# Optimization experiments

Hardware: AMD Instinct MI355X
Metric: run time of the kernel (lower is better)

The kernel has to match this reference:

```python
import jax, jax.numpy as jnp
import numpy as np
from jax import lax

T, B, INPUT_DIM, RNN_DIM = 512, 64, 512, 512
STDV = 1.0 / np.sqrt(float(RNN_DIM))


def setup_inputs() -> dict:
    key = jax.random.key(0)
    k0, k1, k2, k3 = jax.random.split(key, 4)
    input_vectors = jax.random.normal(k0, (T, B, INPUT_DIM), dtype=jnp.float32)
    # params mimic reset_parameters: uniform(-stdv, stdv), stdv = 1/sqrt(rnn_dim)
    weight = jax.random.uniform(k1, (INPUT_DIM + RNN_DIM, RNN_DIM), dtype=jnp.float32, minval=-STDV, maxval=STDV)
    bias = jax.random.uniform(k2, (1, RNN_DIM), dtype=jnp.float32, minval=-STDV, maxval=STDV)
    init_hidden = jax.random.uniform(k3, (1, RNN_DIM), dtype=jnp.float32, minval=-STDV, maxval=STDV)
    return {"input_vectors": input_vectors, "weight": weight, "bias": bias, "init_hidden": init_hidden}


def reference(input_vectors, weight, bias, init_hidden):
    # direction='l'. Output at step i is the hidden state BEFORE the i-th update
    # (the torch code appends prev_hidden before computing new_hidden).
    batch = input_vectors.shape[1]
    rnn_dim = init_hidden.shape[1]
    h0 = jnp.broadcast_to(init_hidden, (batch, rnn_dim))

    def step(h, x):  # h: [B, R], x: [B, D]
        new_h = jnp.tanh(jnp.concatenate([x, h], axis=1) @ weight + bias)
        return new_h, h  # emit pre-update hidden, carry post-update

    _, seq_hidden = lax.scan(step, h0, input_vectors)  # [T, B, R]
    return seq_hidden
```

## Files before the change

### kernel.cpp

```cpp
#include <hip/hip_runtime.h>
#include <hip/hip_bf16.h>
#include <hip/hip_fp16.h>

#define T_STEPS 512
#define BATCH   64
#define DIM     512
#define ROWS    16

typedef _Float16 half2_t __attribute__((ext_vector_type(2)));
typedef _Float16 half8_t __attribute__((ext_vector_type(8)));
typedef short    bf16x8 __attribute__((ext_vector_type(8)));
typedef float    f32x4  __attribute__((ext_vector_type(4)));

static __device__ __forceinline__ unsigned short f2bf(float f) {
    union { float f; unsigned u; } v; v.f = f;
    unsigned r = v.u + 0x7fffu + ((v.u >> 16) & 1u);
    return (unsigned short)(r >> 16);
}

static __device__ __forceinline__ float fast_tanh(float x) {
    float e = __expf(2.0f * x);
    return 1.0f - 2.0f * __builtin_amdgcn_rcpf(e + 1.0f);
}

__global__ __launch_bounds__(256) void tr_cvt_kernel(const float* __restrict__ src,
                                                     unsigned short* __restrict__ dst) {
    __shared__ float tile[32][33];
    const int bx = blockIdx.x * 32;
    const int by = blockIdx.y * 32;
    const int tx = threadIdx.x;
    const int ty = threadIdx.y;
    #pragma unroll
    for (int i = ty; i < 32; i += 8)
        tile[i][tx] = src[(size_t)(by + i) * DIM + (bx + tx)];
    __syncthreads();
    #pragma unroll
    for (int i = ty; i < 32; i += 8)
        dst[(size_t)(bx + i) * DIM + (by + tx)] = f2bf(tile[tx][i]);
}

__global__ __launch_bounds__(256) void tr_cvt_f16_kernel(const float* __restrict__ src,
                                                         _Float16* __restrict__ dst) {
    __shared__ float tile[32][33];
    const int bx = blockIdx.x * 32;
    const int by = blockIdx.y * 32;
    const int tx = threadIdx.x;
    const int ty = threadIdx.y;
    #pragma unroll
    for (int i = ty; i < 32; i += 8)
        tile[i][tx] = src[(size_t)(by + i) * DIM + (bx + tx)];
    __syncthreads();
    #pragma unroll
    for (int i = ty; i < 32; i += 8)
        dst[(size_t)(bx + i) * DIM + (by + tx)] = (_Float16)tile[tx][i];
}

__global__ __launch_bounds__(256) void gemm_z_kernel(const float* __restrict__ X,
                                                     const unsigned short* __restrict__ WxT,
                                                     const float* __restrict__ bias,
                                                     _Float16* __restrict__ Zo) {
    const int bm   = blockIdx.y;
    const int bn   = blockIdx.x;
    const int wave = threadIdx.x >> 6;
    const int lane = threadIdx.x & 63;
    const int mBase = bm * 128 + (wave >> 1) * 64;
    const int nBase = bn * 128 + (wave & 1) * 64;
    const int l15 = lane & 15;
    const int q   = lane >> 4;
    f32x4 acc[4][4] = {};
    for (int kt = 0; kt < 512; kt += 32) {
        const int kk = kt + q * 8;
        bf16x8 a[4], b[4];
        #pragma unroll
        for (int i = 0; i < 4; ++i) {
            const float* ap = X + (size_t)(mBase + i * 16 + l15) * DIM + kk;
            float4 f0 = *(const float4*)(ap);
            float4 f1 = *(const float4*)(ap + 4);
            bf16x8 av;
            av[0] = (short)f2bf(f0.x); av[1] = (short)f2bf(f0.y);
            av[2] = (short)f2bf(f0.z); av[3] = (short)f2bf(f0.w);
            av[4] = (short)f2bf(f1.x); av[5] = (short)f2bf(f1.y);
            av[6] = (short)f2bf(f1.z); av[7] = (short)f2bf(f1.w);
            a[i] = av;
        }
        #pragma unroll
        for (int i = 0; i < 4; ++i)
            b[i] = *(const bf16x8*)(WxT + (size_t)(nBase + i * 16 + l15) * DIM + kk);
        #pragma unroll
        for (int mi = 0; mi < 4; ++mi)
            #pragma unroll
            for (int ni = 0; ni < 4; ++ni)
                acc[mi][ni] = __builtin_amdgcn_mfma_f32_16x16x32_bf16(a[mi], b[ni], acc[mi][ni], 0, 0, 0);
    }
    #pragma unroll
    for (int ni = 0; ni < 4; ++ni) {
        const int col = nBase + ni * 16 + l15;
        const float bv = bias[col];
        const int w_ = col >> 6, ct_ = (col >> 4) & 3, l15_ = col & 15;
        #pragma unroll
        for (int mi = 0; mi < 4; ++mi) {
            #pragma unroll
            for (int rg = 0; rg < 4; ++rg) {
                const int row = mBase + mi * 16 + q * 4 + rg;
                const int t_ = row >> 6, brow = row & 63;
                const int b_ = brow >> 4, r4 = brow & 15;
                const int l_ = (r4 >> 2) * 16 + l15_;
                const int i_ = ct_ * 4 + (r4 & 3);
                Zo[(size_t)t_ * 32768 + (size_t)((b_ * 8 + w_) * 64 + l_) * 16 + i_] =
                    (_Float16)(acc[mi][ni][rg] + bv);
            }
        }
    }
}

__global__ __launch_bounds__(512, 2) void rnn_mfma_kernel(const _Float16* __restrict__ Zw,
                                                          const _Float16* __restrict__ WhT,
                                                          const float* __restrict__ h0,
                                                          float* __restrict__ out) {
    __shared__ _Float16 WlA[65536];
    __shared__ _Float16 Ah[8192];
    const int tid = threadIdx.x;
    const int w = tid >> 6, l = tid & 63;
    const int l15 = l & 15, q = l >> 4;
    const int b = blockIdx.x;
    const int wbase = w * 64;

    half8_t bw[12][4];
    #pragma unroll
    for (int kt = 0; kt < 12; ++kt)
        #pragma unroll
        for (int ct = 0; ct < 4; ++ct)
            bw[kt][ct] = *(const half8_t*)(WhT + (size_t)(wbase + ct * 16 + l15) * DIM + kt * 32 + q * 8);
    #pragma unroll
    for (int kt = 0; kt < 12; ++kt)
        #pragma unroll
        for (int ct = 0; ct < 4; ++ct)
            asm volatile("" : "+v"(bw[kt][ct]));
    #pragma unroll
    for (int ktl = 0; ktl < 4; ++ktl)
        #pragma unroll
        for (int ct = 0; ct < 4; ++ct) {
            half8_t v = *(const half8_t*)(WhT + (size_t)(wbase + ct * 16 + l15) * DIM + (12 + ktl) * 32 + q * 8);
            *(half8_t*)(WlA + (size_t)((w * 16 + ct * 4 + ktl) * 512 + l * 8)) = v;
        }

    const int hi = l15 >> 3, l7 = l15 & 7;
    const int abase = w * 1024 + hi * 32 + q * 8 + l7;
    float* p0 = out + (size_t)(b * 16 + q * 4) * DIM + wbase + l15;
    float h0c[4];
    #pragma unroll
    for (int ct = 0; ct < 4; ++ct) h0c[ct] = h0[wbase + ct * 16 + l15];
    #pragma unroll
    for (int ct = 0; ct < 4; ++ct)
        #pragma unroll
        for (int rg = 0; rg < 4; ++rg) {
            p0[rg * DIM + ct * 16] = h0c[ct];
            Ah[abase + (ct >> 1) * 512 + (ct & 1) * 64 + rg * 128] = (_Float16)h0c[ct];
        }
    __syncthreads();

    const int aslot = (l & 3) * 128 + (l >> 2) * 8;
    const _Float16* pz = Zw + ((size_t)(b * 8 + w) * 64 + l) * 16;
    half8_t z0 = *(const half8_t*)(pz);
    half8_t z1 = *(const half8_t*)(pz + 8);
    float* pout = out + (size_t)(BATCH + b * 16 + q * 4) * DIM + wbase + l15;

    for (int t = 0; t < T_STEPS - 1; ++t) {
        f32x4 acc[4];
        #pragma unroll
        for (int ct = 0; ct < 4; ++ct)
            #pragma unroll
            for (int rg = 0; rg < 4; ++rg) {
                const int i = ct * 4 + rg;
                acc[ct][rg] = (float)(i < 8 ? z0[i] : z1[i - 8]);
            }
        half8_t zn0 = *(const half8_t*)(pz + (size_t)(t + 1) * 32768);
        half8_t zn1 = *(const half8_t*)(pz + (size_t)(t + 1) * 32768 + 8);

        #pragma unroll
        for (int kt = 0; kt < 12; ++kt) {
            half8_t af = *(const half8_t*)(Ah + kt * 512 + aslot);
            #pragma unroll
            for (int ct = 0; ct < 4; ++ct)
                acc[ct] = __builtin_amdgcn_mfma_f32_16x16x32_f16(af, bw[kt][ct], acc[ct], 0, 0, 0);
        }
        #pragma unroll
        for (int ktl = 0; ktl < 4; ++ktl) {
            half8_t af = *(const half8_t*)(Ah + (12 + ktl) * 512 + aslot);
            #pragma unroll
            for (int ct = 0; ct < 4; ++ct) {
                half8_t wf = *(const half8_t*)(WlA + (size_t)((w * 16 + ct * 4 + ktl) * 512 + l * 8));
                acc[ct] = __builtin_amdgcn_mfma_f32_16x16x32_f16(af, wf, acc[ct], 0, 0, 0);
            }
        }
        asm volatile("s_waitcnt lgkmcnt(0)\n\ts_barrier" ::: "memory");
        #pragma unroll
        for (int ct = 0; ct < 4; ++ct)
            #pragma unroll
            for (int rg = 0; rg < 4; ++rg) {
                const float hv = fast_tanh(acc[ct][rg]);
                pout[rg * DIM + ct * 16] = hv;
                Ah[abase + (ct >> 1) * 512 + (ct & 1) * 64 + rg * 128] = (_Float16)hv;
            }
        asm volatile("s_waitcnt lgkmcnt(0)\n\ts_barrier" ::: "memory");
        pout += BATCH * DIM;
        z0 = zn0; z1 = zn1;
    }
}

extern "C" void kernel_launch(void* const* d_in, const int* in_sizes, int n_in,
                              void* d_out, int out_size, void* d_ws, size_t ws_size,
                              hipStream_t stream) {
    const float* X    = (const float*)d_in[0];
    const float* W    = (const float*)d_in[1];
    const float* bias = (const float*)d_in[2];
    const float* h0   = (const float*)d_in[3];
    float* out = (float*)d_out;

    char* ws = (char*)d_ws;
    unsigned short* WxT = (unsigned short*)(ws);
    _Float16*       WhT = (_Float16*)(ws + 524288);
    _Float16*       Zws = (_Float16*)(ws + 1048576);

    dim3 tb(32, 8);
    tr_cvt_kernel<<<dim3(16, 16), tb, 0, stream>>>(W, WxT);
    tr_cvt_f16_kernel<<<dim3(16, 16), tb, 0, stream>>>(W + 512 * 512, WhT);
    gemm_z_kernel<<<dim3(4, 256), 256, 0, stream>>>(X, WxT, bias, Zws);
    rnn_mfma_kernel<<<4, 512, 0, stream>>>(Zws, WhT, h0, out);
}
```

Measured before the change: 1.197 ms.

## Double-buffer hidden state in LDS with XOR swizzle and single barrier per step

The hidden-state LDS buffer is now double-buffered: each step reads from one buffer and writes the new tanh outputs to the other. This removes one of the two workgroup barriers per timestep on the serial recurrence. The A-fragment layout is also changed to an XOR-swizzled slot pattern to reduce LDS bank conflicts, and s_setprio raises wave priority around the MFMA section. In exchange the kernel uses twice the LDS for the hidden state and has more complex address arithmetic.

```diff
diff --git a/kernel.cpp b/kernel.cpp
--- a/kernel.cpp
+++ b/kernel.cpp
@@ -5,7 +5,6 @@
 #define T_STEPS 512
 #define BATCH   64
 #define DIM     512
-#define ROWS    16
 
 typedef _Float16 half2_t __attribute__((ext_vector_type(2)));
 typedef _Float16 half8_t __attribute__((ext_vector_type(8)));
@@ -118,10 +117,11 @@
                                                           const float* __restrict__ h0,
                                                           float* __restrict__ out) {
     __shared__ _Float16 WlA[65536];
-    __shared__ _Float16 Ah[8192];
+    __shared__ _Float16 Ah2[2][8192];
     const int tid = threadIdx.x;
     const int w = tid >> 6, l = tid & 63;
     const int l15 = l & 15, q = l >> 4;
+    const int hi = l15 >> 3, l7 = l15 & 7;
     const int b = blockIdx.x;
     const int wbase = w * 64;
 
@@ -144,28 +144,31 @@
             *(half8_t*)(WlA + (size_t)((w * 16 + ct * 4 + ktl) * 512 + l * 8)) = v;
         }
 
-    const int hi = l15 >> 3, l7 = l15 & 7;
-    const int abase = w * 1024 + hi * 32 + q * 8 + l7;
     float* p0 = out + (size_t)(b * 16 + q * 4) * DIM + wbase + l15;
-    float h0c[4];
-    #pragma unroll
-    for (int ct = 0; ct < 4; ++ct) h0c[ct] = h0[wbase + ct * 16 + l15];
-    #pragma unroll
-    for (int ct = 0; ct < 4; ++ct)
+    #pragma unroll
+    for (int ct = 0; ct < 4; ++ct) {
+        const float hv = h0[wbase + ct * 16 + l15];
+        const int ktc = w * 2 + (ct >> 1);
+        const int Lb  = ((ct & 1) * 2 + hi) * 16 + q * 4;
         #pragma unroll
         for (int rg = 0; rg < 4; ++rg) {
-            p0[rg * DIM + ct * 16] = h0c[ct];
-            Ah[abase + (ct >> 1) * 512 + (ct & 1) * 64 + rg * 128] = (_Float16)h0c[ct];
-        }
+            p0[rg * DIM + ct * 16] = hv;
+            const int L = Lb + rg;
+            const int ps = L ^ (L >> 2);
+            Ah2[0][ktc * 512 + ps * 8 + l7] = (_Float16)hv;
+        }
+    }
     __syncthreads();
 
-    const int aslot = (l & 3) * 128 + (l >> 2) * 8;
+    const int psl = (l ^ (l >> 2)) * 8;
     const _Float16* pz = Zw + ((size_t)(b * 8 + w) * 64 + l) * 16;
     half8_t z0 = *(const half8_t*)(pz);
     half8_t z1 = *(const half8_t*)(pz + 8);
     float* pout = out + (size_t)(BATCH + b * 16 + q * 4) * DIM + wbase + l15;
 
     for (int t = 0; t < T_STEPS - 1; ++t) {
+        const _Float16* Ahr = Ah2[t & 1];
+        _Float16*       Ahw = Ah2[(t + 1) & 1];
         f32x4 acc[4];
         #pragma unroll
         for (int ct = 0; ct < 4; ++ct)
@@ -177,34 +180,51 @@
         half8_t zn0 = *(const half8_t*)(pz + (size_t)(t + 1) * 32768);
         half8_t zn1 = *(const half8_t*)(pz + (size_t)(t + 1) * 32768 + 8);
 
+        __builtin_amdgcn_s_setprio(1);
         #pragma unroll
         for (int kt = 0; kt < 12; ++kt) {
-            half8_t af = *(const half8_t*)(Ah + kt * 512 + aslot);
+            half8_t af = *(const half8_t*)(Ahr + kt * 512 + psl);
             #pragma unroll
             for (int ct = 0; ct < 4; ++ct)
                 acc[ct] = __builtin_amdgcn_mfma_f32_16x16x32_f16(af, bw[kt][ct], acc[ct], 0, 0, 0);
         }
         #pragma unroll
         for (int ktl = 0; ktl < 4; ++ktl) {
-            half8_t af = *(const half8_t*)(Ah + (12 + ktl) * 512 + aslot);
+            half8_t af = *(const half8_t*)(Ahr + (12 + ktl) * 512 + psl);
             #pragma unroll
             for (int ct = 0; ct < 4; ++ct) {
                 half8_t wf = *(const half8_t*)(WlA + (size_t)((w * 16 + ct * 4 + ktl) * 512 + l * 8));
                 acc[ct] = __builtin_amdgcn_mfma_f32_16x16x32_f16(af, wf, acc[ct], 0, 0, 0);
             }
         }
+        __builtin_amdgcn_s_setprio(0);
+
+        float hv[4][4];
+        #pragma unroll
+        for (int ct = 0; ct < 4; ++ct)
+            #pragma unroll
+            for (int rg = 0; rg < 4; ++rg)
+                hv[ct][rg] = fast_tanh(acc[ct][rg]);
+        #pragma unroll
+        for (int ct = 0; ct < 4; ++ct) {
+            const int ktc = w * 2 + (ct >> 1);
+            const int Lb  = ((ct & 1) * 2 + hi) * 16 + q * 4;
+            #pragma unroll
+            for (int rg = 0; rg < 4; ++rg) {
+                const int L = Lb + rg;
+                const int ps = L ^ (L >> 2);
+                Ahw[ktc * 512 + ps * 8 + l7] = (_Float16)hv[ct][rg];
+            }
+        }
+        #pragma unroll
+        for (int ct = 0; ct < 4; ++ct)
+            #pragma unroll
+            for (int rg = 0; rg < 4; ++rg)
+                pout[rg * DIM + ct * 16] = hv[ct][rg];
+
+        z0 = zn0; z1 = zn1;
+        pout += BATCH * DIM;
         asm volatile("s_waitcnt lgkmcnt(0)\n\ts_barrier" ::: "memory");
-        #pragma unroll
-        for (int ct = 0; ct < 4; ++ct)
-            #pragma unroll
-            for (int rg = 0; rg < 4; ++rg) {
-                const float hv = fast_tanh(acc[ct][rg]);
-                pout[rg * DIM + ct * 16] = hv;
-                Ah[abase + (ct >> 1) * 512 + (ct & 1) * 64 + rg * 128] = (_Float16)hv;
-            }
-        asm volatile("s_waitcnt lgkmcnt(0)\n\ts_barrier" ::: "memory");
-        pout += BATCH * DIM;
-        z0 = zn0; z1 = zn1;
     }
 }
 
```

After: 1.306 ms. 1.09x slower.

## Double-buffer hidden state, swap MFMA operands, stream weight tail from global

Applied to the files above, without the earlier changes.

Double-buffers the fp16 hidden-state LDS tile so each step needs one barrier instead of two. It also swaps the MFMA operand order so each lane holds four consecutive output columns, which allows vectorized float4 output stores and half4 LDS writes with an XOR-swizzled layout. The last four K tiles of the recurrent weight are now re-read from global/L2 every step instead of from a large LDS copy, and a dummy LDS pad limits occupancy. It also raises wave priority around the MFMA chain, adding per-step global weight traffic in exchange for less LDS use and fewer syncs.

```diff
diff --git a/kernel.cpp b/kernel.cpp
--- a/kernel.cpp
+++ b/kernel.cpp
@@ -5,9 +5,11 @@
 #define T_STEPS 512
 #define BATCH   64
 #define DIM     512
-#define ROWS    16
+#define REG_KT  12
+#define STR_KT  4
 
 typedef _Float16 half2_t __attribute__((ext_vector_type(2)));
+typedef _Float16 half4_t __attribute__((ext_vector_type(4)));
 typedef _Float16 half8_t __attribute__((ext_vector_type(8)));
 typedef short    bf16x8 __attribute__((ext_vector_type(8)));
 typedef float    f32x4  __attribute__((ext_vector_type(4)));
@@ -96,17 +98,19 @@
     for (int ni = 0; ni < 4; ++ni) {
         const int col = nBase + ni * 16 + l15;
         const float bv = bias[col];
-        const int w_ = col >> 6, ct_ = (col >> 4) & 3, l15_ = col & 15;
+        const int w_  = col >> 6;
+        const int c64 = col & 63;
+        const int ct_ = c64 >> 4;
+        const int q_  = (c64 & 15) >> 2;
+        const int rg_ = c64 & 3;
         #pragma unroll
         for (int mi = 0; mi < 4; ++mi) {
             #pragma unroll
             for (int rg = 0; rg < 4; ++rg) {
                 const int row = mBase + mi * 16 + q * 4 + rg;
-                const int t_ = row >> 6, brow = row & 63;
-                const int b_ = brow >> 4, r4 = brow & 15;
-                const int l_ = (r4 >> 2) * 16 + l15_;
-                const int i_ = ct_ * 4 + (r4 & 3);
-                Zo[(size_t)t_ * 32768 + (size_t)((b_ * 8 + w_) * 64 + l_) * 16 + i_] =
+                const int t_ = row >> 6, batch = row & 63;
+                const int b_ = batch >> 4, l15k = batch & 15;
+                Zo[(size_t)t_ * 32768 + (size_t)((b_ * 8 + w_) * 64 + (q_ * 16 + l15k)) * 16 + ct_ * 4 + rg_] =
                     (_Float16)(acc[mi][ni][rg] + bv);
             }
         }
@@ -117,55 +121,63 @@
                                                           const _Float16* __restrict__ WhT,
                                                           const float* __restrict__ h0,
                                                           float* __restrict__ out) {
-    __shared__ _Float16 WlA[65536];
-    __shared__ _Float16 Ah[8192];
+    __shared__ _Float16 Ah2[2][8192];
+    __shared__ half8_t  lds_pad[3600];
     const int tid = threadIdx.x;
     const int w = tid >> 6, l = tid & 63;
     const int l15 = l & 15, q = l >> 4;
     const int b = blockIdx.x;
     const int wbase = w * 64;
 
-    half8_t bw[12][4];
-    #pragma unroll
-    for (int kt = 0; kt < 12; ++kt)
+    ((volatile _Float16*)lds_pad)[tid] = (_Float16)0.f;
+
+    half8_t bw[REG_KT][4];
+    #pragma unroll
+    for (int kt = 0; kt < REG_KT; ++kt)
         #pragma unroll
         for (int ct = 0; ct < 4; ++ct)
             bw[kt][ct] = *(const half8_t*)(WhT + (size_t)(wbase + ct * 16 + l15) * DIM + kt * 32 + q * 8);
     #pragma unroll
-    for (int kt = 0; kt < 12; ++kt)
+    for (int kt = 0; kt < REG_KT; ++kt)
         #pragma unroll
         for (int ct = 0; ct < 4; ++ct)
             asm volatile("" : "+v"(bw[kt][ct]));
-    #pragma unroll
-    for (int ktl = 0; ktl < 4; ++ktl)
-        #pragma unroll
-        for (int ct = 0; ct < 4; ++ct) {
-            half8_t v = *(const half8_t*)(WhT + (size_t)(wbase + ct * 16 + l15) * DIM + (12 + ktl) * 32 + q * 8);
-            *(half8_t*)(WlA + (size_t)((w * 16 + ct * 4 + ktl) * 512 + l * 8)) = v;
-        }
-
-    const int hi = l15 >> 3, l7 = l15 & 7;
-    const int abase = w * 1024 + hi * 32 + q * 8 + l7;
-    float* p0 = out + (size_t)(b * 16 + q * 4) * DIM + wbase + l15;
-    float h0c[4];
-    #pragma unroll
-    for (int ct = 0; ct < 4; ++ct) h0c[ct] = h0[wbase + ct * 16 + l15];
+
+    const _Float16* pw[4];
     #pragma unroll
     for (int ct = 0; ct < 4; ++ct)
-        #pragma unroll
-        for (int rg = 0; rg < 4; ++rg) {
-            p0[rg * DIM + ct * 16] = h0c[ct];
-            Ah[abase + (ct >> 1) * 512 + (ct & 1) * 64 + rg * 128] = (_Float16)h0c[ct];
-        }
+        pw[ct] = WhT + (size_t)(wbase + ct * 16 + l15) * DIM + REG_KT * 32 + q * 8;
+
+    int aw_off[4];
+    #pragma unroll
+    for (int ct = 0; ct < 4; ++ct) {
+        const int kt = w * 2 + (ct >> 1);
+        const int Lt = ((ct & 1) * 2 + (q >> 1)) * 16 + l15;
+        const int ps = Lt ^ (Lt >> 2);
+        aw_off[ct] = kt * 512 + ps * 8 + (q & 1) * 4;
+    }
+
+    float* p0 = out + (size_t)(b * 16 + l15) * DIM + wbase + q * 4;
+    #pragma unroll
+    for (int ct = 0; ct < 4; ++ct) {
+        const float4 hv = *(const float4*)(h0 + wbase + ct * 16 + q * 4);
+        *(float4*)(p0 + ct * 16) = hv;
+        half4_t hh;
+        hh[0] = (_Float16)hv.x; hh[1] = (_Float16)hv.y;
+        hh[2] = (_Float16)hv.z; hh[3] = (_Float16)hv.w;
+        *(half4_t*)(&Ah2[0][0] + aw_off[ct]) = hh;
+    }
     __syncthreads();
 
-    const int aslot = (l & 3) * 128 + (l >> 2) * 8;
+    const int psl = (l ^ (l >> 2)) * 8;
     const _Float16* pz = Zw + ((size_t)(b * 8 + w) * 64 + l) * 16;
     half8_t z0 = *(const half8_t*)(pz);
     half8_t z1 = *(const half8_t*)(pz + 8);
-    float* pout = out + (size_t)(BATCH + b * 16 + q * 4) * DIM + wbase + l15;
+    float* pout = out + (size_t)(BATCH + b * 16 + l15) * DIM + wbase + q * 4;
 
     for (int t = 0; t < T_STEPS - 1; ++t) {
+        const _Float16* Ahr = Ah2[t & 1];
+        _Float16*       Ahw = Ah2[(t + 1) & 1];
         f32x4 acc[4];
         #pragma unroll
         for (int ct = 0; ct < 4; ++ct)
@@ -176,35 +188,47 @@
             }
         half8_t zn0 = *(const half8_t*)(pz + (size_t)(t + 1) * 32768);
         half8_t zn1 = *(const half8_t*)(pz + (size_t)(t + 1) * 32768 + 8);
-
-        #pragma unroll
-        for (int kt = 0; kt < 12; ++kt) {
-            half8_t af = *(const half8_t*)(Ah + kt * 512 + aslot);
+        half8_t sw[STR_KT][4];
+        #pragma unroll
+        for (int ktl = 0; ktl < STR_KT; ++ktl)
             #pragma unroll
             for (int ct = 0; ct < 4; ++ct)
-                acc[ct] = __builtin_amdgcn_mfma_f32_16x16x32_f16(af, bw[kt][ct], acc[ct], 0, 0, 0);
-        }
-        #pragma unroll
-        for (int ktl = 0; ktl < 4; ++ktl) {
-            half8_t af = *(const half8_t*)(Ah + (12 + ktl) * 512 + aslot);
-            #pragma unroll
-            for (int ct = 0; ct < 4; ++ct) {
-                half8_t wf = *(const half8_t*)(WlA + (size_t)((w * 16 + ct * 4 + ktl) * 512 + l * 8));
-                acc[ct] = __builtin_amdgcn_mfma_f32_16x16x32_f16(af, wf, acc[ct], 0, 0, 0);
-            }
-        }
+                sw[ktl][ct] = *(const half8_t*)(pw[ct] + ktl * 32);
+
+        __builtin_amdgcn_s_setprio(1);
+        #pragma unroll
+        for (int kt = 0; kt < REG_KT; ++kt) {
+            half8_t hf = *(const half8_t*)(Ahr + kt * 512 + psl);
+            #pragma unroll
+            for (int ct = 0; ct < 4; ++ct)
+                acc[ct] = __builtin_amdgcn_mfma_f32_16x16x32_f16(bw[kt][ct], hf, acc[ct], 0, 0, 0);
+        }
+        #pragma unroll
+        for (int ktl = 0; ktl < STR_KT; ++ktl) {
+            half8_t hf = *(const half8_t*)(Ahr + (REG_KT + ktl) * 512 + psl);
+            #pragma unroll
+            for (int ct = 0; ct < 4; ++ct)
+                acc[ct] = __builtin_amdgcn_mfma_f32_16x16x32_f16(sw[ktl][ct], hf, acc[ct], 0, 0, 0);
+        }
+        __builtin_amdgcn_s_setprio(0);
+
+        #pragma unroll
+        for (int ct = 0; ct < 4; ++ct) {
+            float4 hv;
+            hv.x = fast_tanh(acc[ct][0]);
+            hv.y = fast_tanh(acc[ct][1]);
+            hv.z = fast_tanh(acc[ct][2]);
+            hv.w = fast_tanh(acc[ct][3]);
+            half4_t hh;
+            hh[0] = (_Float16)hv.x; hh[1] = (_Float16)hv.y;
+            hh[2] = (_Float16)hv.z; hh[3] = (_Float16)hv.w;
+            *(half4_t*)(Ahw + aw_off[ct]) = hh;
+            *(float4*)(pout + ct * 16) = hv;
+        }
+
+        z0 = zn0; z1 = zn1;
+        pout += BATCH * DIM;
         asm volatile("s_waitcnt lgkmcnt(0)\n\ts_barrier" ::: "memory");
-        #pragma unroll
-        for (int ct = 0; ct < 4; ++ct)
-            #pragma unroll
-            for (int rg = 0; rg < 4; ++rg) {
-                const float hv = fast_tanh(acc[ct][rg]);
-                pout[rg * DIM + ct * 16] = hv;
-                Ah[abase + (ct >> 1) * 512 + (ct & 1) * 64 + rg * 128] = (_Float16)hv;
-            }
-        asm volatile("s_waitcnt lgkmcnt(0)\n\ts_barrier" ::: "memory");
-        pout += BATCH * DIM;
-        z0 = zn0; z1 = zn1;
     }
 }
 
```

Result: slower. 2.401 ms (+100.6%).
